# Kernel tuning notes

Hardware: AMD Instinct MI355X
Metric: run time of the kernel (lower is better)

The kernel has to match this reference:

```python
import jax, jax.numpy as jnp
import numpy as np

EPS = 1e-12  # tf.math.l2_normalize default epsilon

def _l2_normalize(x, axis):
    sq = jnp.sum(x * x, axis=axis, keepdims=True)
    return x * jax.lax.rsqrt(jnp.maximum(sq, EPS))

def setup_inputs() -> dict:
    key = jax.random.key(0)
    k1, k2 = jax.random.split(key)
    B, L, D, K = 4096, 200, 64, 8
    inputs = jax.random.normal(k1, (B, L, D), dtype=jnp.float32)
    prototype = jax.random.normal(k2, (K, D), dtype=jnp.float32)
    return {"inputs": inputs, "prototype": prototype}

def reference(inputs, prototype):
    # inputs: [B, L, D], prototype: [K, D]
    normed_interests = _l2_normalize(inputs, axis=-1)      # [B, L, D]
    normed_prototype = _l2_normalize(prototype, axis=-1)   # [K, D]
    # cosine_sim: [B, K, L] = prototype @ interests^T (broadcast over batch)
    cosine_sim = jnp.einsum('kd,bld->bkl', normed_prototype, normed_interests)
    # softmax over the slot/prototype axis K (axis=-2)
    attn = jax.nn.softmax(cosine_sim, axis=-2)              # [B, K, L]
    # projected interests: [B, K, D]
    return jnp.einsum('bkl,bld->bkd', attn, inputs)
```

## Files before the change

### kernel.cpp

```cpp
#include <hip/hip_runtime.h>


#define LQ 200
#define DQ 64
#define KQ 8
#define NSTEP 25

typedef float v2f __attribute__((ext_vector_type(2)));

__device__ __forceinline__ float dppx1(float v) {
    return __int_as_float(__builtin_amdgcn_update_dpp(0, __float_as_int(v), 0xB1, 0xF, 0xF, true));
}
__device__ __forceinline__ float dppx2(float v) {
    return __int_as_float(__builtin_amdgcn_update_dpp(0, __float_as_int(v), 0x4E, 0xF, 0xF, true));
}
__device__ __forceinline__ float xor4(float v) {
    int vi = __float_as_int(v);
    int r1 = __builtin_amdgcn_update_dpp(0,  vi, 0x104, 0xF, 0x5, false);
    int r  = __builtin_amdgcn_update_dpp(r1, vi, 0x114, 0xF, 0xA, false);
    return __int_as_float(r);
}
__device__ __forceinline__ float allred8(float v) {
    v += dppx1(v); v += dppx2(v); v += xor4(v); return v;
}
__device__ __forceinline__ v2f fma2(v2f a, v2f b, v2f c) {
    return __builtin_elementwise_fma(a, b, c);
}
__device__ __forceinline__ float hsum2(v2f v) { return v.x + v.y; }

__device__ __forceinline__ float reduce_dots(const float* s, bool b1, bool b2, bool b3) {
    float T0 = (b1 ? s[1] : s[0]) + dppx1(b1 ? s[0] : s[1]);
    float T1 = (b1 ? s[3] : s[2]) + dppx1(b1 ? s[2] : s[3]);
    float T2 = (b1 ? s[5] : s[4]) + dppx1(b1 ? s[4] : s[5]);
    float T3 = (b1 ? s[7] : s[6]) + dppx1(b1 ? s[6] : s[7]);
    float K0 = (b2 ? T1 : T0) + dppx2(b2 ? T0 : T1);
    float K1 = (b2 ? T3 : T2) + dppx2(b2 ? T2 : T3);
    return (b3 ? K1 : K0) + xor4(b3 ? K0 : K1);
}

struct Ctx {
    float4 pA[KQ], pB[KQ];
    float rnp;
    bool b1, b2, b3;
};

__device__ __forceinline__ void step_compute(float4 f0, float4 f1,
                                             const Ctx& cx, v2f (&acc)[KQ][4]) {
    v2f x0 = {f0.x, f0.y}, x1 = {f0.z, f0.w};
    v2f x2 = {f1.x, f1.y}, x3 = {f1.z, f1.w};

    float s[KQ];
    #pragma unroll
    for (int k = 0; k < KQ; ++k) {
        v2f pa0 = {cx.pA[k].x, cx.pA[k].y}, pa1 = {cx.pA[k].z, cx.pA[k].w};
        v2f pb0 = {cx.pB[k].x, cx.pB[k].y}, pb1 = {cx.pB[k].z, cx.pB[k].w};
        v2f t2 = fma2(x3, pb1, fma2(x2, pb0, fma2(x1, pa1, x0 * pa0)));
        s[k] = hsum2(t2);
    }
    float d = reduce_dots(s, cx.b1, cx.b2, cx.b3) * cx.rnp;

    v2f q2 = fma2(x3, x3, fma2(x2, x2, fma2(x1, x1, x0 * x0)));
    float sq = allred8(hsum2(q2));

    float e0 = __expf(d * __builtin_amdgcn_rsqf(fmaxf(sq, 1e-12f)));
    float e1 = dppx1(e0);
    float e2 = dppx2(e0);
    float e3 = dppx2(e1);
    float e4 = xor4(e0);
    float e5 = xor4(e1);
    float e6 = xor4(e2);
    float e7 = xor4(e3);
    float rd = __builtin_amdgcn_rcpf(((e0 + e1) + (e2 + e3)) + ((e4 + e5) + (e6 + e7)));
    float aj[KQ] = {e0 * rd, e1 * rd, e2 * rd, e3 * rd,
                    e4 * rd, e5 * rd, e6 * rd, e7 * rd};

    #pragma unroll
    for (int j = 0; j < KQ; ++j) {
        v2f aa = {aj[j], aj[j]};
        acc[j][0] = fma2(aa, x0, acc[j][0]);
        acc[j][1] = fma2(aa, x1, acc[j][1]);
        acc[j][2] = fma2(aa, x2, acc[j][2]);
        acc[j][3] = fma2(aa, x3, acc[j][3]);
    }
}

__global__ __launch_bounds__(64, 2) void projector_kernel(const float* __restrict__ x,
                                                          const float* __restrict__ proto,
                                                          float* __restrict__ out) {
    const int b = blockIdx.x;
    const int t = threadIdx.x;
    const int c = t & 7;
    const int a = t >> 3;

    Ctx cx;
    cx.b1 = (c & 1) != 0;
    cx.b2 = (c & 2) != 0;
    cx.b3 = (c & 4) != 0;

    const float4* p4  = (const float4*)proto;
    const float4* xb4 = (const float4*)(x + (size_t)b * (LQ * DQ));

    #pragma unroll
    for (int k = 0; k < KQ; ++k) {
        cx.pA[k] = p4[k * 16 + 2 * c];
        cx.pB[k] = p4[k * 16 + 2 * c + 1];
    }
    {
        float sp[KQ];
        #pragma unroll
        for (int k = 0; k < KQ; ++k) {
            v2f a0 = {cx.pA[k].x, cx.pA[k].y}, a1 = {cx.pA[k].z, cx.pA[k].w};
            v2f b0 = {cx.pB[k].x, cx.pB[k].y}, b1v = {cx.pB[k].z, cx.pB[k].w};
            sp[k] = hsum2(fma2(b1v, b1v, fma2(b0, b0, fma2(a1, a1, a0 * a0))));
        }
        cx.rnp = __builtin_amdgcn_rsqf(fmaxf(reduce_dots(sp, cx.b1, cx.b2, cx.b3), 1e-12f));
    }

    v2f acc[KQ][4];
    #pragma unroll
    for (int j = 0; j < KQ; ++j)
        #pragma unroll
        for (int q = 0; q < 4; ++q) acc[j][q] = (v2f){0.f, 0.f};

    const int lofs = a * 16 + 2 * c;

    float4 s0a = xb4[0 * 128 + lofs], s0b = xb4[0 * 128 + lofs + 1];
    float4 s1a = xb4[1 * 128 + lofs], s1b = xb4[1 * 128 + lofs + 1];
    float4 s2a = xb4[2 * 128 + lofs], s2b = xb4[2 * 128 + lofs + 1];
    float4 s3a = xb4[3 * 128 + lofs], s3b = xb4[3 * 128 + lofs + 1];

    #pragma unroll 1
    for (int g = 0; g < 6; ++g) {
        const int base = 4 * g;
        {
            const int sn = (base + 4 < NSTEP) ? base + 4 : NSTEP - 1;
            float4 na = xb4[sn * 128 + lofs], nb = xb4[sn * 128 + lofs + 1];
            step_compute(s0a, s0b, cx, acc);
            s0a = na; s0b = nb;
        }
        {
            const int sn = (base + 5 < NSTEP) ? base + 5 : NSTEP - 1;
            float4 na = xb4[sn * 128 + lofs], nb = xb4[sn * 128 + lofs + 1];
            step_compute(s1a, s1b, cx, acc);
            s1a = na; s1b = nb;
        }
        {
            const int sn = (base + 6 < NSTEP) ? base + 6 : NSTEP - 1;
            float4 na = xb4[sn * 128 + lofs], nb = xb4[sn * 128 + lofs + 1];
            step_compute(s2a, s2b, cx, acc);
            s2a = na; s2b = nb;
        }
        {
            const int sn = (base + 7 < NSTEP) ? base + 7 : NSTEP - 1;
            float4 na = xb4[sn * 128 + lofs], nb = xb4[sn * 128 + lofs + 1];
            step_compute(s3a, s3b, cx, acc);
            s3a = na; s3b = nb;
        }
    }
    step_compute(s0a, s0b, cx, acc);

    #pragma unroll
    for (int i = 0; i < 4; ++i)
        #pragma unroll
        for (int q = 0; q < 4; ++q) {
            v2f send = (a & 1) ? acc[i][q] : acc[i + 4][q];
            v2f keep = (a & 1) ? acc[i + 4][q] : acc[i][q];
            v2f r = {__shfl_xor(send.x, 8, 64), __shfl_xor(send.y, 8, 64)};
            acc[i][q] = keep + r;
        }
    #pragma unroll
    for (int i = 0; i < 2; ++i)
        #pragma unroll
        for (int q = 0; q < 4; ++q) {
            v2f send = (a & 2) ? acc[i][q] : acc[i + 2][q];
            v2f keep = (a & 2) ? acc[i + 2][q] : acc[i][q];
            v2f r = {__shfl_xor(send.x, 16, 64), __shfl_xor(send.y, 16, 64)};
            acc[i][q] = keep + r;
        }
    #pragma unroll
    for (int q = 0; q < 4; ++q) {
        v2f send = (a & 4) ? acc[0][q] : acc[1][q];
        v2f keep = (a & 4) ? acc[1][q] : acc[0][q];
        v2f r = {__shfl_xor(send.x, 32, 64), __shfl_xor(send.y, 32, 64)};
        acc[0][q] = keep + r;
    }

    const int j = ((a & 1) << 2) | (a & 2) | ((a & 4) >> 2);
    const int k = c ^ j;
    float4* og = (float4*)(out + (size_t)b * (KQ * DQ));
    og[k * 16 + 2 * c]     = make_float4(acc[0][0].x, acc[0][0].y, acc[0][1].x, acc[0][1].y);
    og[k * 16 + 2 * c + 1] = make_float4(acc[0][2].x, acc[0][2].y, acc[0][3].x, acc[0][3].y);
}

extern "C" void kernel_launch(void* const* d_in, const int* in_sizes, int n_in,
                              void* d_out, int out_size, void* d_ws, size_t ws_size,
                              hipStream_t stream) {
    const float* x     = (const float*)d_in[0];
    const float* proto = (const float*)d_in[1];
    float* out = (float*)d_out;

    const int Bn = in_sizes[0] / (LQ * DQ);

    projector_kernel<<<Bn, 64, 0, stream>>>(x, proto, out);
}
```

Baseline: 43.54 us.

## Split prototypes across lane halves to cut registers and double occupancy

Each row of the input is now handled by two 8-lane groups, each owning 4 of the 8 prototypes, so each wave covers 4 rows per step over 50 steps. This halves the accumulator and prototype registers per lane, and the launch bounds rise from 2 to 4 waves per SIMD to hide memory latency. The softmax denominator is completed across the two halves with a new cross-8-lane DPP exchange, and the output reduction loses one shuffle stage. In exchange, every row is loaded by both groups and its squared norm and exp are computed twice.

```diff
diff --git a/kernel.cpp b/kernel.cpp
--- a/kernel.cpp
+++ b/kernel.cpp
@@ -4,7 +4,7 @@
 #define LQ 200
 #define DQ 64
 #define KQ 8
-#define NSTEP 25
+#define NSTEP 50
 
 typedef float v2f __attribute__((ext_vector_type(2)));
 
@@ -20,6 +20,12 @@
     int r  = __builtin_amdgcn_update_dpp(r1, vi, 0x114, 0xF, 0xA, false);
     return __int_as_float(r);
 }
+__device__ __forceinline__ float xor8(float v) {
+    int vi = __float_as_int(v);
+    int r1 = __builtin_amdgcn_update_dpp(0,  vi, 0x108, 0xF, 0x3, false);
+    int r  = __builtin_amdgcn_update_dpp(r1, vi, 0x118, 0xF, 0xC, false);
+    return __int_as_float(r);
+}
 __device__ __forceinline__ float allred8(float v) {
     v += dppx1(v); v += dppx2(v); v += xor4(v); return v;
 }
@@ -28,36 +34,32 @@
 }
 __device__ __forceinline__ float hsum2(v2f v) { return v.x + v.y; }
 
-__device__ __forceinline__ float reduce_dots(const float* s, bool b1, bool b2, bool b3) {
+__device__ __forceinline__ float reduce4(const float* s, bool b1, bool b2) {
     float T0 = (b1 ? s[1] : s[0]) + dppx1(b1 ? s[0] : s[1]);
     float T1 = (b1 ? s[3] : s[2]) + dppx1(b1 ? s[2] : s[3]);
-    float T2 = (b1 ? s[5] : s[4]) + dppx1(b1 ? s[4] : s[5]);
-    float T3 = (b1 ? s[7] : s[6]) + dppx1(b1 ? s[6] : s[7]);
-    float K0 = (b2 ? T1 : T0) + dppx2(b2 ? T0 : T1);
-    float K1 = (b2 ? T3 : T2) + dppx2(b2 ? T2 : T3);
-    return (b3 ? K1 : K0) + xor4(b3 ? K0 : K1);
+    float K  = (b2 ? T1 : T0) + dppx2(b2 ? T0 : T1);
+    return K + xor4(K);
 }
 
 struct Ctx {
-    float4 pA[KQ], pB[KQ];
+    float4 pA[4], pB[4];
     float rnp;
-    bool b1, b2, b3;
+    bool b1, b2;
 };
 
 __device__ __forceinline__ void step_compute(float4 f0, float4 f1,
-                                             const Ctx& cx, v2f (&acc)[KQ][4]) {
+                                             const Ctx& cx, v2f (&acc)[4][4]) {
     v2f x0 = {f0.x, f0.y}, x1 = {f0.z, f0.w};
     v2f x2 = {f1.x, f1.y}, x3 = {f1.z, f1.w};
 
-    float s[KQ];
+    float s[4];
     #pragma unroll
-    for (int k = 0; k < KQ; ++k) {
-        v2f pa0 = {cx.pA[k].x, cx.pA[k].y}, pa1 = {cx.pA[k].z, cx.pA[k].w};
-        v2f pb0 = {cx.pB[k].x, cx.pB[k].y}, pb1 = {cx.pB[k].z, cx.pB[k].w};
-        v2f t2 = fma2(x3, pb1, fma2(x2, pb0, fma2(x1, pa1, x0 * pa0)));
-        s[k] = hsum2(t2);
+    for (int j = 0; j < 4; ++j) {
+        v2f pa0 = {cx.pA[j].x, cx.pA[j].y}, pa1 = {cx.pA[j].z, cx.pA[j].w};
+        v2f pb0 = {cx.pB[j].x, cx.pB[j].y}, pb1 = {cx.pB[j].z, cx.pB[j].w};
+        s[j] = hsum2(fma2(x3, pb1, fma2(x2, pb0, fma2(x1, pa1, x0 * pa0))));
     }
-    float d = reduce_dots(s, cx.b1, cx.b2, cx.b3) * cx.rnp;
+    float d = reduce4(s, cx.b1, cx.b2) * cx.rnp;
 
     v2f q2 = fma2(x3, x3, fma2(x2, x2, fma2(x1, x1, x0 * x0)));
     float sq = allred8(hsum2(q2));
@@ -66,127 +68,111 @@
     float e1 = dppx1(e0);
     float e2 = dppx2(e0);
     float e3 = dppx2(e1);
-    float e4 = xor4(e0);
-    float e5 = xor4(e1);
-    float e6 = xor4(e2);
-    float e7 = xor4(e3);
-    float rd = __builtin_amdgcn_rcpf(((e0 + e1) + (e2 + e3)) + ((e4 + e5) + (e6 + e7)));
-    float aj[KQ] = {e0 * rd, e1 * rd, e2 * rd, e3 * rd,
-                    e4 * rd, e5 * rd, e6 * rd, e7 * rd};
+    float qs  = (e0 + e1) + (e2 + e3);
+    float den = qs + xor8(qs);
+    float rd  = __builtin_amdgcn_rcpf(den);
+    float a0 = e0 * rd, a1 = e1 * rd, a2 = e2 * rd, a3 = e3 * rd;
 
-    #pragma unroll
-    for (int j = 0; j < KQ; ++j) {
-        v2f aa = {aj[j], aj[j]};
-        acc[j][0] = fma2(aa, x0, acc[j][0]);
-        acc[j][1] = fma2(aa, x1, acc[j][1]);
-        acc[j][2] = fma2(aa, x2, acc[j][2]);
-        acc[j][3] = fma2(aa, x3, acc[j][3]);
+    {
+        v2f aa = {a0, a0};
+        acc[0][0] = fma2(aa, x0, acc[0][0]); acc[0][1] = fma2(aa, x1, acc[0][1]);
+        acc[0][2] = fma2(aa, x2, acc[0][2]); acc[0][3] = fma2(aa, x3, acc[0][3]);
+    }
+    {
+        v2f aa = {a1, a1};
+        acc[1][0] = fma2(aa, x0, acc[1][0]); acc[1][1] = fma2(aa, x1, acc[1][1]);
+        acc[1][2] = fma2(aa, x2, acc[1][2]); acc[1][3] = fma2(aa, x3, acc[1][3]);
+    }
+    {
+        v2f aa = {a2, a2};
+        acc[2][0] = fma2(aa, x0, acc[2][0]); acc[2][1] = fma2(aa, x1, acc[2][1]);
+        acc[2][2] = fma2(aa, x2, acc[2][2]); acc[2][3] = fma2(aa, x3, acc[2][3]);
+    }
+    {
+        v2f aa = {a3, a3};
+        acc[3][0] = fma2(aa, x0, acc[3][0]); acc[3][1] = fma2(aa, x1, acc[3][1]);
+        acc[3][2] = fma2(aa, x2, acc[3][2]); acc[3][3] = fma2(aa, x3, acc[3][3]);
     }
 }
 
-__global__ __launch_bounds__(64, 2) void projector_kernel(const float* __restrict__ x,
+__global__ __launch_bounds__(64, 4) void projector_kernel(const float* __restrict__ x,
                                                           const float* __restrict__ proto,
                                                           float* __restrict__ out) {
     const int b = blockIdx.x;
     const int t = threadIdx.x;
     const int c = t & 7;
-    const int a = t >> 3;
+    const int h = (t >> 3) & 1;
+    const int r = t >> 4;
 
     Ctx cx;
     cx.b1 = (c & 1) != 0;
     cx.b2 = (c & 2) != 0;
-    cx.b3 = (c & 4) != 0;
 
     const float4* p4  = (const float4*)proto;
     const float4* xb4 = (const float4*)(x + (size_t)b * (LQ * DQ));
 
     #pragma unroll
-    for (int k = 0; k < KQ; ++k) {
-        cx.pA[k] = p4[k * 16 + 2 * c];
-        cx.pB[k] = p4[k * 16 + 2 * c + 1];
+    for (int j = 0; j < 4; ++j) {
+        cx.pA[j] = p4[(h * 4 + j) * 16 + 2 * c];
+        cx.pB[j] = p4[(h * 4 + j) * 16 + 2 * c + 1];
     }
     {
-        float sp[KQ];
+        float sp[4];
         #pragma unroll
-        for (int k = 0; k < KQ; ++k) {
-            v2f a0 = {cx.pA[k].x, cx.pA[k].y}, a1 = {cx.pA[k].z, cx.pA[k].w};
-            v2f b0 = {cx.pB[k].x, cx.pB[k].y}, b1v = {cx.pB[k].z, cx.pB[k].w};
-            sp[k] = hsum2(fma2(b1v, b1v, fma2(b0, b0, fma2(a1, a1, a0 * a0))));
+        for (int j = 0; j < 4; ++j) {
+            v2f a0 = {cx.pA[j].x, cx.pA[j].y}, a1 = {cx.pA[j].z, cx.pA[j].w};
+            v2f b0 = {cx.pB[j].x, cx.pB[j].y}, b1v = {cx.pB[j].z, cx.pB[j].w};
+            sp[j] = hsum2(fma2(b1v, b1v, fma2(b0, b0, fma2(a1, a1, a0 * a0))));
         }
-        cx.rnp = __builtin_amdgcn_rsqf(fmaxf(reduce_dots(sp, cx.b1, cx.b2, cx.b3), 1e-12f));
+        cx.rnp = __builtin_amdgcn_rsqf(fmaxf(reduce4(sp, cx.b1, cx.b2), 1e-12f));
     }
 
-    v2f acc[KQ][4];
+    v2f acc[4][4];
     #pragma unroll
-    for (int j = 0; j < KQ; ++j)
+    for (int m = 0; m < 4; ++m)
         #pragma unroll
-        for (int q = 0; q < 4; ++q) acc[j][q] = (v2f){0.f, 0.f};
+        for (int q = 0; q < 4; ++q) acc[m][q] = (v2f){0.f, 0.f};
 
-    const int lofs = a * 16 + 2 * c;
+    const int l0 = r * 16 + 2 * c;
 
-    float4 s0a = xb4[0 * 128 + lofs], s0b = xb4[0 * 128 + lofs + 1];
-    float4 s1a = xb4[1 * 128 + lofs], s1b = xb4[1 * 128 + lofs + 1];
-    float4 s2a = xb4[2 * 128 + lofs], s2b = xb4[2 * 128 + lofs + 1];
-    float4 s3a = xb4[3 * 128 + lofs], s3b = xb4[3 * 128 + lofs + 1];
+    float4 aA = xb4[l0],      aB = xb4[l0 + 1];
+    float4 bA = xb4[64 + l0], bB = xb4[64 + l0 + 1];
 
     #pragma unroll 1
-    for (int g = 0; g < 6; ++g) {
-        const int base = 4 * g;
+    for (int g = 0; g < 25; ++g) {
+        int s2 = 2 * g + 2; s2 = (s2 < NSTEP) ? s2 : NSTEP - 1;
+        int s3 = 2 * g + 3; s3 = (s3 < NSTEP) ? s3 : NSTEP - 1;
         {
-            const int sn = (base + 4 < NSTEP) ? base + 4 : NSTEP - 1;
-            float4 na = xb4[sn * 128 + lofs], nb = xb4[sn * 128 + lofs + 1];
-            step_compute(s0a, s0b, cx, acc);
-            s0a = na; s0b = nb;
+            float4 na = xb4[s2 * 64 + l0], nb = xb4[s2 * 64 + l0 + 1];
+            step_compute(aA, aB, cx, acc);
+            aA = na; aB = nb;
         }
         {
-            const int sn = (base + 5 < NSTEP) ? base + 5 : NSTEP - 1;
-            float4 na = xb4[sn * 128 + lofs], nb = xb4[sn * 128 + lofs + 1];
-            step_compute(s1a, s1b, cx, acc);
-            s1a = na; s1b = nb;
-        }
-        {
-            const int sn = (base + 6 < NSTEP) ? base + 6 : NSTEP - 1;
-            float4 na = xb4[sn * 128 + lofs], nb = xb4[sn * 128 + lofs + 1];
-            step_compute(s2a, s2b, cx, acc);
-            s2a = na; s2b = nb;
-        }
-        {
-            const int sn = (base + 7 < NSTEP) ? base + 7 : NSTEP - 1;
-            float4 na = xb4[sn * 128 + lofs], nb = xb4[sn * 128 + lofs + 1];
-            step_compute(s3a, s3b, cx, acc);
-            s3a = na; s3b = nb;
+            float4 na = xb4[s3 * 64 + l0], nb = xb4[s3 * 64 + l0 + 1];
+            step_compute(bA, bB, cx, acc);
+            bA = na; bB = nb;
         }
     }
-    step_compute(s0a, s0b, cx, acc);
 
-    #pragma unroll
-    for (int i = 0; i < 4; ++i)
-        #pragma unroll
-        for (int q = 0; q < 4; ++q) {
-            v2f send = (a & 1) ? acc[i][q] : acc[i + 4][q];
-            v2f keep = (a & 1) ? acc[i + 4][q] : acc[i][q];
-            v2f r = {__shfl_xor(send.x, 8, 64), __shfl_xor(send.y, 8, 64)};
-            acc[i][q] = keep + r;
-        }
     #pragma unroll
     for (int i = 0; i < 2; ++i)
         #pragma unroll
         for (int q = 0; q < 4; ++q) {
-            v2f send = (a & 2) ? acc[i][q] : acc[i + 2][q];
-            v2f keep = (a & 2) ? acc[i + 2][q] : acc[i][q];
-            v2f r = {__shfl_xor(send.x, 16, 64), __shfl_xor(send.y, 16, 64)};
-            acc[i][q] = keep + r;
+            v2f send = (r & 1) ? acc[i][q] : acc[i + 2][q];
+            v2f keep = (r & 1) ? acc[i + 2][q] : acc[i][q];
+            v2f rr = {__shfl_xor(send.x, 16, 64), __shfl_xor(send.y, 16, 64)};
+            acc[i][q] = keep + rr;
         }
     #pragma unroll
     for (int q = 0; q < 4; ++q) {
-        v2f send = (a & 4) ? acc[0][q] : acc[1][q];
-        v2f keep = (a & 4) ? acc[1][q] : acc[0][q];
-        v2f r = {__shfl_xor(send.x, 32, 64), __shfl_xor(send.y, 32, 64)};
-        acc[0][q] = keep + r;
+        v2f send = (r & 2) ? acc[0][q] : acc[1][q];
+        v2f keep = (r & 2) ? acc[1][q] : acc[0][q];
+        v2f rr = {__shfl_xor(send.x, 32, 64), __shfl_xor(send.y, 32, 64)};
+        acc[0][q] = keep + rr;
     }
 
-    const int j = ((a & 1) << 2) | (a & 2) | ((a & 4) >> 2);
-    const int k = c ^ j;
+    const int m = 2 * (r & 1) + ((r >> 1) & 1);
+    const int k = h * 4 + ((c & 3) ^ m);
     float4* og = (float4*)(out + (size_t)b * (KQ * DQ));
     og[k * 16 + 2 * c]     = make_float4(acc[0][0].x, acc[0][0].y, acc[0][1].x, acc[0][1].y);
     og[k * 16 + 2 * c + 1] = make_float4(acc[0][2].x, acc[0][2].y, acc[0][3].x, acc[0][3].y);
```

After: 50.51 us. +16.0%, slower.
